# Kernel optimization log

Measured on AMD Instinct MI355X. Metric: run time of the kernel, lower is better.

The kernel has to match this reference:

```python
import jax, jax.numpy as jnp
import numpy as np

PI = float(np.pi)

def setup_inputs() -> dict:
    key = jax.random.key(0)
    k1, k2 = jax.random.split(key)
    inp = jax.random.normal(k1, (16, 4096, 512), dtype=jnp.float32)
    lengths = jax.random.randint(k2, (16,), 0, 4096, dtype=jnp.int32)
    return {"inp": inp, "lengths": lengths}

def reference(inp, lengths):
    B, S, D = inp.shape
    pos = jnp.arange(S, dtype=jnp.float32)                      # [S]
    lens = lengths.astype(jnp.float32)[:, None]                  # [B,1]
    safe_len = jnp.maximum(lens, 1.0)
    # cos(x / len * pi) for x < len, else 0 (matches torch.zeros init)
    pe = jnp.where(pos[None, :] < lens,
                   jnp.cos(pos[None, :] / safe_len * PI),
                   0.0)                                          # [B,S]
    pe = pe.astype(inp.dtype)
    # original intent: concatenate positional channel along feature dim
    return jnp.concatenate([inp, pe[:, :, None]], axis=2)        # [B,S,D+1]
```

## Files before the change

kernel.cpp:

```cpp
#include <hip/hip_runtime.h>
#include <math.h>


#define PS   4096
#define PD   512
#define PDO  513
#define PI_F 3.14159265358979323846f
#define OUT_V4 8404992
#define IN_V4  8388608
#define TPB  256
#define CPT  4

__global__ __launch_bounds__(TPB) void sinpe_kernel(
    const float* __restrict__ inp,
    const int* __restrict__ lengths,
    float* __restrict__ out)
{
    const float4* __restrict__ in4  = (const float4*)inp;
    float4* __restrict__       out4 = (float4*)out;

    const int q0 = blockIdx.x * (TPB * CPT) + threadIdx.x;

    float4 cur[CPT], prv[CPT];
    int r_[CPT], c0_[CPT];

#pragma unroll
    for (int k = 0; k < CPT; ++k) {
        const int q  = q0 + k * TPB;
        const int l0 = q << 2;
        const int r  = (int)__umulhi((unsigned)l0, 8372256u);
        const int c0 = l0 - r * PDO;
        const int sh = r >> 2;
        const int si = q - sh;
        int ci = si;     if (ci > IN_V4 - 1) ci = IN_V4 - 1;
        int pi = si - 1; if (pi < 0)         pi = 0;
        cur[k] = in4[ci];
        prv[k] = in4[pi];
        r_[k] = r; c0_[k] = c0;
    }

#pragma unroll
    for (int k = 0; k < CPT; ++k) {
        const int q   = q0 + k * TPB;
        const int r   = r_[k];
        const int c0  = c0_[k];
        const int dlt = r & 3;

        const float px = prv[k].x, py = prv[k].y, pz = prv[k].z, pw = prv[k].w;
        const float cx = cur[k].x, cy = cur[k].y, cz = cur[k].z, cw = cur[k].w;
        const bool d2 = (dlt & 2) != 0;
        const bool d1 = (dlt & 1) != 0;
        const float Am1 = d2 ? py : pw;
        const float A0  = d2 ? pz : cx;
        const float A1  = d2 ? pw : cy;
        const float A2  = d2 ? cx : cz;
        const float A3  = d2 ? cy : cw;
        float w0 = d1 ? Am1 : A0;
        float w1 = d1 ? A0  : A1;
        float w2 = d1 ? A1  : A2;
        float w3 = d1 ? A2  : A3;

        if (c0 >= 509) {
            const int mpe = 512 - c0;
            const int b   = r >> 12;
            const int s   = r & (PS - 1);
            const int len = lengths[b];
            float pe = 0.0f;
            if (s < len)
                pe = cosf(((float)s / fmaxf((float)len, 1.0f)) * PI_F);
            const float n0 = (mpe == 0) ? pe : w0;
            const float n1 = (mpe == 1) ? pe : ((mpe < 1) ? w0 : w1);
            const float n2 = (mpe == 2) ? pe : ((mpe < 2) ? w1 : w2);
            const float n3 = (mpe == 3) ? pe : w2;
            w0 = n0; w1 = n1; w2 = n2; w3 = n3;
        }

        float4 o;
        o.x = w0; o.y = w1; o.z = w2; o.w = w3;
        out4[q] = o;
    }
}

extern "C" void kernel_launch(void* const* d_in, const int* in_sizes, int n_in,
                              void* d_out, int out_size, void* d_ws, size_t ws_size,
                              hipStream_t stream)
{
    const float* inp     = (const float*)d_in[0];
    const int*   lengths = (const int*)d_in[1];
    float*       out     = (float*)d_out;

    const int n_blocks = OUT_V4 / (TPB * CPT);
    sinpe_kernel<<<n_blocks, TPB, 0, stream>>>(inp, lengths, out);
}
```

Before: 232.0 us.

## Use persistent grid-stride loop with software-prefetched chunks and nontemporal stores

Replaces the one-shot grid of blocks, each handling four float4 chunks per thread, with a fixed 2048-block persistent grid. Each thread loops over the output with a grid stride and prefetches the next two chunks while processing the current two. Output writes become nontemporal stores to cut cache pollution on the streaming write. The loop adds bounds checks and register pressure, and the fixed grid size may underfill or imbalance the device.

```diff
diff --git a/kernel.cpp b/kernel.cpp
--- a/kernel.cpp
+++ b/kernel.cpp
@@ -3,81 +3,112 @@
 
 
 #define PS   4096
-#define PD   512
 #define PDO  513
 #define PI_F 3.14159265358979323846f
 #define OUT_V4 8404992
 #define IN_V4  8388608
-#define TPB  256
-#define CPT  4
+#define TPB   256
+#define NBLK  2048
+#define ISTR  (2 * TPB * NBLK)
+#define NITER ((OUT_V4 + ISTR - 1) / ISTR)
+
+typedef float f32x4 __attribute__((ext_vector_type(4)));
+
+struct Chunk { f32x4 cur, prv; int r, c0; };
+
+__device__ __forceinline__ void load_chunk(const f32x4* __restrict__ in4,
+                                           int q, Chunk& ch)
+{
+    const int l0 = q << 2;
+    const int r  = (int)__umulhi((unsigned)l0, 8372256u);
+    const int c0 = l0 - r * PDO;
+    const int si = q - (r >> 2);
+    int ci = si;     if (ci > IN_V4 - 1) ci = IN_V4 - 1;
+    int pi = si - 1; if (pi < 0)         pi = 0;
+    ch.cur = in4[ci];
+    ch.prv = in4[pi];
+    ch.r = r; ch.c0 = c0;
+}
+
+__device__ __forceinline__ f32x4 funnel(const Chunk& ch,
+                                        const int* __restrict__ lengths)
+{
+    const int r   = ch.r;
+    const int c0  = ch.c0;
+    const int dlt = r & 3;
+
+    const float px = ch.prv.x, py = ch.prv.y, pz = ch.prv.z, pw = ch.prv.w;
+    const float cx = ch.cur.x, cy = ch.cur.y, cz = ch.cur.z, cw = ch.cur.w;
+    const bool d2 = (dlt & 2) != 0;
+    const bool d1 = (dlt & 1) != 0;
+    const float Am1 = d2 ? py : pw;
+    const float A0  = d2 ? pz : cx;
+    const float A1  = d2 ? pw : cy;
+    const float A2  = d2 ? cx : cz;
+    const float A3  = d2 ? cy : cw;
+    float w0 = d1 ? Am1 : A0;
+    float w1 = d1 ? A0  : A1;
+    float w2 = d1 ? A1  : A2;
+    float w3 = d1 ? A2  : A3;
+
+    if (c0 >= 509) {
+        const int mpe = 512 - c0;
+        const int b   = r >> 12;
+        const int s   = r & (PS - 1);
+        const int len = lengths[b];
+        float pe = 0.0f;
+        if (s < len)
+            pe = cosf(((float)s / fmaxf((float)len, 1.0f)) * PI_F);
+        const float n0 = (mpe == 0) ? pe : w0;
+        const float n1 = (mpe == 1) ? pe : ((mpe < 1) ? w0 : w1);
+        const float n2 = (mpe == 2) ? pe : ((mpe < 2) ? w1 : w2);
+        const float n3 = (mpe == 3) ? pe : w2;
+        w0 = n0; w1 = n1; w2 = n2; w3 = n3;
+    }
+
+    f32x4 o;
+    o.x = w0; o.y = w1; o.z = w2; o.w = w3;
+    return o;
+}
 
 __global__ __launch_bounds__(TPB) void sinpe_kernel(
     const float* __restrict__ inp,
     const int* __restrict__ lengths,
     float* __restrict__ out)
 {
-    const float4* __restrict__ in4  = (const float4*)inp;
-    float4* __restrict__       out4 = (float4*)out;
+    const f32x4* __restrict__ in4  = (const f32x4*)inp;
+    f32x4* __restrict__       out4 = (f32x4*)out;
 
-    const int q0 = blockIdx.x * (TPB * CPT) + threadIdx.x;
+    int base = blockIdx.x * (2 * TPB) + threadIdx.x;
 
-    float4 cur[CPT], prv[CPT];
-    int r_[CPT], c0_[CPT];
+    Chunk A, B;
+    load_chunk(in4, min(base, OUT_V4 - 1), A);
+    load_chunk(in4, min(base + TPB, OUT_V4 - 1), B);
 
-#pragma unroll
-    for (int k = 0; k < CPT; ++k) {
-        const int q  = q0 + k * TPB;
-        const int l0 = q << 2;
-        const int r  = (int)__umulhi((unsigned)l0, 8372256u);
-        const int c0 = l0 - r * PDO;
-        const int sh = r >> 2;
-        const int si = q - sh;
-        int ci = si;     if (ci > IN_V4 - 1) ci = IN_V4 - 1;
-        int pi = si - 1; if (pi < 0)         pi = 0;
-        cur[k] = in4[ci];
-        prv[k] = in4[pi];
-        r_[k] = r; c0_[k] = c0;
-    }
+#pragma unroll 1
+    for (int i = 0; i < NITER; ++i) {
+        const int qa = base;
+        const int qb = base + TPB;
+        const int nb = base + ISTR;
 
-#pragma unroll
-    for (int k = 0; k < CPT; ++k) {
-        const int q   = q0 + k * TPB;
-        const int r   = r_[k];
-        const int c0  = c0_[k];
-        const int dlt = r & 3;
-
-        const float px = prv[k].x, py = prv[k].y, pz = prv[k].z, pw = prv[k].w;
-        const float cx = cur[k].x, cy = cur[k].y, cz = cur[k].z, cw = cur[k].w;
-        const bool d2 = (dlt & 2) != 0;
-        const bool d1 = (dlt & 1) != 0;
-        const float Am1 = d2 ? py : pw;
-        const float A0  = d2 ? pz : cx;
-        const float A1  = d2 ? pw : cy;
-        const float A2  = d2 ? cx : cz;
-        const float A3  = d2 ? cy : cw;
-        float w0 = d1 ? Am1 : A0;
-        float w1 = d1 ? A0  : A1;
-        float w2 = d1 ? A1  : A2;
-        float w3 = d1 ? A2  : A3;
-
-        if (c0 >= 509) {
-            const int mpe = 512 - c0;
-            const int b   = r >> 12;
-            const int s   = r & (PS - 1);
-            const int len = lengths[b];
-            float pe = 0.0f;
-            if (s < len)
-                pe = cosf(((float)s / fmaxf((float)len, 1.0f)) * PI_F);
-            const float n0 = (mpe == 0) ? pe : w0;
-            const float n1 = (mpe == 1) ? pe : ((mpe < 1) ? w0 : w1);
-            const float n2 = (mpe == 2) ? pe : ((mpe < 2) ? w1 : w2);
-            const float n3 = (mpe == 3) ? pe : w2;
-            w0 = n0; w1 = n1; w2 = n2; w3 = n3;
+        Chunk nA, nB;
+        if (i + 1 < NITER) {
+            load_chunk(in4, min(nb, OUT_V4 - 1), nA);
+            load_chunk(in4, min(nb + TPB, OUT_V4 - 1), nB);
+        } else {
+            nA = A; nB = B;
         }
 
-        float4 o;
-        o.x = w0; o.y = w1; o.z = w2; o.w = w3;
-        out4[q] = o;
+        if (qa < OUT_V4) {
+            f32x4 o = funnel(A, lengths);
+            __builtin_nontemporal_store(o, &out4[qa]);
+        }
+        if (qb < OUT_V4) {
+            f32x4 o = funnel(B, lengths);
+            __builtin_nontemporal_store(o, &out4[qb]);
+        }
+
+        A = nA; B = nB; base = nb;
     }
 }
 
@@ -89,6 +120,5 @@
     const int*   lengths = (const int*)d_in[1];
     float*       out     = (float*)d_out;
 
-    const int n_blocks = OUT_V4 / (TPB * CPT);
-    sinpe_kernel<<<n_blocks, TPB, 0, stream>>>(inp, lengths, out);
+    sinpe_kernel<<<NBLK, TPB, 0, stream>>>(inp, lengths, out);
 }
```

Result: slower. 241.1 us (+3.9%).
